# Kernel optimization log

Hardware: AMD Instinct MI355X
Metric: run time of the kernel (lower is better)

The kernel has to match this reference:

```python
import jax, jax.numpy as jnp
import numpy as np

B, T, D = 8, 1024, 768
H, DH = 12, 64
E, K, DFF = 16, 2, 3072
EPS = 1e-5


def _ln(x, w, b):
    m = x.mean(-1, keepdims=True)
    v = ((x - m) ** 2).mean(-1, keepdims=True)
    return (x - m) * jax.lax.rsqrt(v + EPS) * w + b


def setup_inputs() -> dict:
    key = jax.random.key(0)
    ks = jax.random.split(key, 12)
    s = 0.02
    return {
        "x": jax.random.normal(ks[0], (B, T, D), jnp.float32),
        "ln1_w": jnp.ones((D,), jnp.float32),
        "ln1_b": jnp.zeros((D,), jnp.float32),
        "qkv_w": jax.random.normal(ks[1], (D, 3 * D), jnp.float32) * s,
        "qkv_b": jnp.zeros((3 * D,), jnp.float32),
        "proj_w": jax.random.normal(ks[2], (D, D), jnp.float32) * s,
        "proj_b": jnp.zeros((D,), jnp.float32),
        "ln2_w": jnp.ones((D,), jnp.float32),
        "ln2_b": jnp.zeros((D,), jnp.float32),
        "router_w": jax.random.normal(ks[3], (D, E), jnp.float32) * s,
        "w1": jax.random.normal(ks[4], (E, D, DFF), jnp.float32) * s,
        "b1": jnp.zeros((E, DFF), jnp.float32),
        "w2": jax.random.normal(ks[5], (E, DFF, D), jnp.float32) * s,
        "b2": jnp.zeros((E, D), jnp.float32),
    }


def _block(x, ln1_w, ln1_b, qkv_w, qkv_b, proj_w, proj_b,
           ln2_w, ln2_b, router_w, w1, b1, w2, b2):
    # --- attention ---
    h = _ln(x, ln1_w, ln1_b)
    qkv = h @ qkv_w + qkv_b                      # [B,T,3D]
    q, k, v = jnp.split(qkv, 3, axis=-1)
    q = q.reshape(B, T, H, DH).transpose(0, 2, 1, 3)
    k = k.reshape(B, T, H, DH).transpose(0, 2, 1, 3)
    v = v.reshape(B, T, H, DH).transpose(0, 2, 1, 3)
    scores = jnp.einsum("bhqd,bhkd->bhqk", q, k) / np.sqrt(DH)
    causal = jnp.tril(jnp.ones((T, T), bool))
    scores = jnp.where(causal, scores, -jnp.inf)
    attn = jax.nn.softmax(scores, axis=-1)
    y = jnp.einsum("bhqk,bhkd->bhqd", attn, v)
    y = y.transpose(0, 2, 1, 3).reshape(B, T, D)
    x = x + y @ proj_w + proj_b                  # residual 1

    # --- MoE FFN (dense all-experts, gated combine) ---
    z = _ln(x, ln2_w, ln2_b)                     # [B,T,D]
    probs = jax.nn.softmax(z @ router_w, axis=-1)  # [B,T,E]
    top_p, ix = jax.lax.top_k(probs, K)
    gate = (jax.nn.one_hot(ix, E, dtype=probs.dtype) * top_p[..., None]).sum(-2)  # [B,T,E]
    gate_e = jnp.moveaxis(gate, -1, 0)           # [E,B,T]

    def body(acc, ew):
        g, W1, B1, W2, B2 = ew
        out = jax.nn.gelu(z @ W1 + B1, approximate=False) @ W2 + B2
        return acc + g[..., None] * out, None

    yff, _ = jax.lax.scan(body, jnp.zeros_like(z), (gate_e, w1, b1, w2, b2))
    # MoELayer returns z + yff; Block adds x again (faithful double residual)
    return x + z + yff


def reference(x, ln1_w, ln1_b, qkv_w, qkv_b, proj_w, proj_b,
              ln2_w, ln2_b, router_w, w1, b1, w2, b2):
    return _block(x, ln1_w, ln1_b, qkv_w, qkv_b, proj_w, proj_b,
                  ln2_w, ln2_b, router_w, w1, b1, w2, b2)
```

## Files before the change

kernel.cpp:

```cpp
#include <hip/hip_runtime.h>
#include <math.h>

#define D_MODEL 768
#define T_SEQ   1024
#define B_BATCH 8
#define NTOK    8192
#define H_HEADS 12
#define DHEAD   64
#define NEXP    16
#define DFF     3072
#define NPAIR   16384
#define MAXT128 144
#define MAXT256 80

typedef unsigned short u16;
typedef unsigned int   u32;

typedef __attribute__((ext_vector_type(8))) short bf16x8;
typedef __attribute__((ext_vector_type(4))) float f32x4;
typedef __attribute__((ext_vector_type(4))) u32   u32x4;

__device__ __forceinline__ float bf2f(u16 u) { return __uint_as_float(((u32)u) << 16); }
__device__ __forceinline__ u16 f2bf(float f) {
    u32 u = __float_as_uint(f);
    return (u16)((u + 0x7FFFu + ((u >> 16) & 1u)) >> 16);
}

__device__ __forceinline__ void gload16(const void* g, void* l) {
    __builtin_amdgcn_global_load_lds((const __attribute__((address_space(1))) void*)g,
                                     (__attribute__((address_space(3))) void*)l, 16, 0, 0);
}

__global__ __launch_bounds__(256) void ln_kernel(const float* __restrict__ x,
                                                 const float* __restrict__ w,
                                                 const float* __restrict__ b,
                                                 u16* __restrict__ out_bf,
                                                 float* __restrict__ out_f) {
    const int row = blockIdx.x;
    const int tid = threadIdx.x;
    const float* xr = x + (size_t)row * D_MODEL;
    float v0 = xr[tid], v1 = xr[tid + 256], v2 = xr[tid + 512];
    float s = v0 + v1 + v2;
    float s2 = v0 * v0 + v1 * v1 + v2 * v2;
#pragma unroll
    for (int o = 32; o > 0; o >>= 1) { s += __shfl_down(s, o); s2 += __shfl_down(s2, o); }
    __shared__ float red[8];
    __shared__ float stats[2];
    const int wid = tid >> 6;
    if ((tid & 63) == 0) { red[wid] = s; red[4 + wid] = s2; }
    __syncthreads();
    if (tid == 0) {
        float ts = red[0] + red[1] + red[2] + red[3];
        float ts2 = red[4] + red[5] + red[6] + red[7];
        float mean = ts * (1.0f / D_MODEL);
        float var = ts2 * (1.0f / D_MODEL) - mean * mean;
        stats[0] = mean;
        stats[1] = rsqrtf(var + 1e-5f);
    }
    __syncthreads();
    const float mean = stats[0], rstd = stats[1];
    u16* orow = out_bf + (size_t)row * D_MODEL;
    float r0 = (v0 - mean) * rstd * w[tid]       + b[tid];
    float r1 = (v1 - mean) * rstd * w[tid + 256] + b[tid + 256];
    float r2 = (v2 - mean) * rstd * w[tid + 512] + b[tid + 512];
    orow[tid] = f2bf(r0); orow[tid + 256] = f2bf(r1); orow[tid + 512] = f2bf(r2);
    if (out_f) {
        float* frow = out_f + (size_t)row * D_MODEL;
        frow[tid] = r0; frow[tid + 256] = r1; frow[tid + 512] = r2;
    }
}

__global__ __launch_bounds__(256) void transpose_cvt(const float* __restrict__ src,
                                                     u16* __restrict__ dst,
                                                     int R, int C) {
    const size_t plane = (size_t)R * C;
    src += (size_t)blockIdx.z * plane;
    dst += (size_t)blockIdx.z * plane;
    __shared__ __align__(16) u16 tile[64][72];
    const int t = threadIdx.x;
    const int r0 = blockIdx.y * 64, c0 = blockIdx.x * 64;
    {
        const int lr = t >> 2, lc = (t & 3) * 16;
        const float* sp = src + (size_t)(r0 + lr) * C + c0 + lc;
        u16 tmp[16];
#pragma unroll
        for (int j = 0; j < 4; ++j) {
            f32x4 f = *(const f32x4*)(sp + j * 4);
            tmp[j * 4 + 0] = f2bf(f[0]); tmp[j * 4 + 1] = f2bf(f[1]);
            tmp[j * 4 + 2] = f2bf(f[2]); tmp[j * 4 + 3] = f2bf(f[3]);
        }
        *(u32x4*)&tile[lr][lc]     = *(const u32x4*)&tmp[0];
        *(u32x4*)&tile[lr][lc + 8] = *(const u32x4*)&tmp[8];
    }
    __syncthreads();
    {
        const int ln = t >> 2, lk0 = (t & 3) * 16;
        u16 o[16];
#pragma unroll
        for (int j = 0; j < 16; ++j) o[j] = tile[lk0 + j][ln];
        u16* d = dst + (size_t)(c0 + ln) * R + r0 + lk0;
        *(u32x4*)&d[0] = *(const u32x4*)&o[0];
        *(u32x4*)&d[8] = *(const u32x4*)&o[8];
    }
}

template <int MODE>
__global__ __launch_bounds__(512, 4) void gemm256(
    const u16* __restrict__ A, const u16* __restrict__ Bt,
    const float* __restrict__ bias, void* __restrict__ Cout,
    const float* __restrict__ resid,
    const int* __restrict__ bucket_tok, const int* __restrict__ offsets,
    const int* __restrict__ counts, const int* __restrict__ desc_e,
    const int* __restrict__ desc_r, const int* __restrict__ tile_cnt,
    int K, int N)
{
    int e = 0, r0 = 0, off = 0, ne = 0, row0 = 0;
    const int col0 = blockIdx.x * 128;
    if constexpr (MODE >= 2) {
        if ((int)blockIdx.y >= *tile_cnt) return;
        e = desc_e[blockIdx.y];
        r0 = desc_r[blockIdx.y];
        off = offsets[e];
        ne = counts[e];
    } else {
        row0 = blockIdx.y * 256;
    }
    if constexpr (MODE == 2) Bt += (size_t)e * D_MODEL * DFF;
    if constexpr (MODE == 3) Bt += (size_t)e * DFF * D_MODEL;

    __shared__ __align__(16) u16 As[256 * 64];
    __shared__ __align__(16) u16 Bs[128 * 64];

    const int tid = threadIdx.x;
    const int lane = tid & 63;
    const int w = tid >> 6;
    const int wm = w >> 1, wn = w & 1;
    const int fr = lane & 15, fg = lane >> 4;

    const int koff = ((((tid & 7) * 16) ^ (((tid >> 3) & 7) << 4)) >> 1);

    u32 aoff[4];
#pragma unroll
    for (int i = 0; i < 4; ++i) {
        const int r = i * 64 + (tid >> 3);
        u32 row;
        if constexpr (MODE == 2) {
            int rb = r0 + r;
            row = (u32)bucket_tok[off + (rb < ne ? rb : 0)];
        } else if constexpr (MODE == 3) {
            int rb = r0 + r;
            row = (u32)(off + (rb < ne ? rb : (ne - 1)));
        } else {
            row = (u32)(row0 + r);
        }
        aoff[i] = row * (u32)K + (u32)koff;
    }
    u32 boff[2];
#pragma unroll
    for (int i = 0; i < 2; ++i) {
        const int n = i * 64 + (tid >> 3);
        boff[i] = (u32)(col0 + n) * (u32)K + (u32)koff;
    }

    f32x4 acc[4][4] = {};

    for (int k0 = 0; k0 < K; k0 += 64) {
        __syncthreads();
#pragma unroll
        for (int i = 0; i < 4; ++i)
            gload16(A + aoff[i] + k0, &As[(i * 512 + w * 64) * 8]);
#pragma unroll
        for (int i = 0; i < 2; ++i)
            gload16(Bt + boff[i] + k0, &Bs[(i * 512 + w * 64) * 8]);
        __syncthreads();
#pragma unroll
        for (int kk = 0; kk < 2; ++kk) {
            const int sw = ((kk * 64 + fg * 16) ^ ((fr & 7) << 4)) >> 1;
            bf16x8 a[4], b[4];
#pragma unroll
            for (int mi = 0; mi < 4; ++mi)
                a[mi] = *(const bf16x8*)&As[(wm * 64 + mi * 16 + fr) * 64 + sw];
#pragma unroll
            for (int ni = 0; ni < 4; ++ni)
                b[ni] = *(const bf16x8*)&Bs[(wn * 64 + ni * 16 + fr) * 64 + sw];
#pragma unroll
            for (int mi = 0; mi < 4; ++mi)
#pragma unroll
                for (int ni = 0; ni < 4; ++ni)
                    acc[mi][ni] = __builtin_amdgcn_mfma_f32_16x16x32_bf16(a[mi], b[ni], acc[mi][ni], 0, 0, 0);
        }
    }

#pragma unroll
    for (int mi = 0; mi < 4; ++mi) {
#pragma unroll
        for (int ni = 0; ni < 4; ++ni) {
            const int lr = wm * 64 + mi * 16 + fg * 4;
            const int col = col0 + wn * 64 + ni * 16 + fr;
#pragma unroll
            for (int i = 0; i < 4; ++i) {
                float v = acc[mi][ni][i];
                if constexpr (MODE == 0) {
                    int grow = row0 + lr + i;
                    ((u16*)Cout)[(size_t)grow * N + col] = f2bf(v + bias[col]);
                } else if constexpr (MODE == 1) {
                    int grow = row0 + lr + i;
                    size_t idx = (size_t)grow * N + col;
                    ((float*)Cout)[idx] = resid[idx] + v + bias[col];
                } else if constexpr (MODE == 2) {
                    int rb = r0 + lr + i;
                    if (rb < ne) {
                        float vb = v + bias[(size_t)e * DFF + col];
                        float g = 0.5f * vb * (1.0f + erff(vb * 0.70710678118654752f));
                        ((u16*)Cout)[(size_t)(off + rb) * N + col] = f2bf(g);
                    }
                } else {
                    int rb = r0 + lr + i;
                    if (rb < ne) {
                        ((float*)Cout)[(size_t)(off + rb) * N + col] = v + bias[(size_t)e * D_MODEL + col];
                    }
                }
            }
        }
    }
}

template <int MODE>
__global__ __launch_bounds__(256) void gemm128f(
    const u16* __restrict__ A, const float* __restrict__ Bf,
    const float* __restrict__ bias, void* __restrict__ Cout,
    const float* __restrict__ resid,
    const int* __restrict__ bucket_tok, const int* __restrict__ offsets,
    const int* __restrict__ counts, const int* __restrict__ desc_e,
    const int* __restrict__ desc_r, const int* __restrict__ tile_cnt,
    int K, int N)
{
    int e = 0, r0 = 0, off = 0, ne = 0, row0 = 0;
    const int col0 = blockIdx.x * 128;
    if constexpr (MODE >= 2) {
        if ((int)blockIdx.y >= *tile_cnt) return;
        e = desc_e[blockIdx.y]; r0 = desc_r[blockIdx.y];
        off = offsets[e]; ne = counts[e];
    } else row0 = blockIdx.y * 128;
    if constexpr (MODE == 2) Bf += (size_t)e * D_MODEL * DFF;
    if constexpr (MODE == 3) Bf += (size_t)e * DFF * D_MODEL;

    __shared__ __align__(16) u16 AsL[128 * 32];
    __shared__ __align__(16) u16 BsL[128 * 32];

    const int tid = threadIdx.x;
    const int lane = tid & 63;
    const int w = tid >> 6;
    const int wr = (w >> 1) * 64, wc = (w & 1) * 64;
    const int fr = lane & 15, fg = lane >> 4;
    const int lrow = lane >> 2, lk = (lane & 3) * 8;

    const u16* ag[2];
#pragma unroll
    for (int i = 0; i < 2; ++i) {
        int r = i * 64 + w * 16 + lrow;
        size_t srow;
        if constexpr (MODE == 2) {
            int rb = r0 + r;
            int tok = bucket_tok[off + (rb < ne ? rb : 0)];
            srow = (size_t)tok * K;
        } else if constexpr (MODE == 3) {
            int rb = r0 + r;
            int pp = off + (rb < ne ? rb : (ne - 1));
            srow = (size_t)pp * K;
        } else srow = (size_t)(row0 + r) * K;
        ag[i] = A + srow + lk;
    }

    f32x4 acc[4][4] = {};
    for (int k0 = 0; k0 < K; k0 += 32) {
        __syncthreads();
        gload16(ag[0] + k0, &AsL[0 * 2048 + w * 512]);
        gload16(ag[1] + k0, &AsL[1 * 2048 + w * 512]);
#pragma unroll
        for (int i = 0; i < 4; ++i) {
            int s = tid + 256 * i;
            int kk = s >> 5, n4 = (s & 31) * 4;
            f32x4 f = *(const f32x4*)(Bf + (size_t)(k0 + kk) * N + col0 + n4);
            BsL[(n4 + 0) * 32 + kk] = f2bf(f[0]);
            BsL[(n4 + 1) * 32 + kk] = f2bf(f[1]);
            BsL[(n4 + 2) * 32 + kk] = f2bf(f[2]);
            BsL[(n4 + 3) * 32 + kk] = f2bf(f[3]);
        }
        __syncthreads();
        bf16x8 a[4], b[4];
#pragma unroll
        for (int mi = 0; mi < 4; ++mi)
            a[mi] = *(const bf16x8*)&AsL[(wr + mi * 16 + fr) * 32 + fg * 8];
#pragma unroll
        for (int ni = 0; ni < 4; ++ni)
            b[ni] = *(const bf16x8*)&BsL[(wc + ni * 16 + fr) * 32 + fg * 8];
#pragma unroll
        for (int mi = 0; mi < 4; ++mi)
#pragma unroll
            for (int ni = 0; ni < 4; ++ni)
                acc[mi][ni] = __builtin_amdgcn_mfma_f32_16x16x32_bf16(a[mi], b[ni], acc[mi][ni], 0, 0, 0);
    }
#pragma unroll
    for (int mi = 0; mi < 4; ++mi) {
#pragma unroll
        for (int ni = 0; ni < 4; ++ni) {
            const int lr = wr + mi * 16 + fg * 4;
            const int col = col0 + wc + ni * 16 + fr;
#pragma unroll
            for (int i = 0; i < 4; ++i) {
                float v = acc[mi][ni][i];
                if constexpr (MODE == 0) {
                    int grow = row0 + lr + i;
                    ((u16*)Cout)[(size_t)grow * N + col] = f2bf(v + bias[col]);
                } else if constexpr (MODE == 1) {
                    int grow = row0 + lr + i;
                    size_t idx = (size_t)grow * N + col;
                    ((float*)Cout)[idx] = resid[idx] + v + bias[col];
                } else if constexpr (MODE == 2) {
                    int rb = r0 + lr + i;
                    if (rb < ne) {
                        float vb = v + bias[(size_t)e * DFF + col];
                        float g = 0.5f * vb * (1.0f + erff(vb * 0.70710678118654752f));
                        ((u16*)Cout)[(size_t)(off + rb) * N + col] = f2bf(g);
                    }
                } else {
                    int rb = r0 + lr + i;
                    if (rb < ne) {
                        ((float*)Cout)[(size_t)(off + rb) * N + col] = v + bias[(size_t)e * D_MODEL + col];
                    }
                }
            }
        }
    }
}

__global__ __launch_bounds__(256) void attn_mfma(const u16* __restrict__ qkv,
                                                 u16* __restrict__ y) {
    const int bh = blockIdx.x;
    const int b = bh / H_HEADS, h = bh % H_HEADS;
    const int qt = gridDim.y - 1 - blockIdx.y;
    const int tid = threadIdx.x, lane = tid & 63, w = tid >> 6;
    const int fr = lane & 15, fg = lane >> 4;

    __shared__ __align__(16) u16 Ks[64][72];
    __shared__ __align__(16) u16 Vt[64][72];
    __shared__ __align__(16) u16 Ps[4][16][72];

    const int tb = b * T_SEQ + qt * 64;

    bf16x8 aq[2];
    {
        const u16* qp = qkv + (size_t)(tb + w * 16 + fr) * (3 * D_MODEL) + h * DHEAD + fg * 8;
        aq[0] = *(const bf16x8*)qp;
        aq[1] = *(const bf16x8*)(qp + 32);
    }
    f32x4 accO[4] = {};
    float m_[4], l_[4];
#pragma unroll
    for (int i = 0; i < 4; ++i) { m_[i] = -1e30f; l_[i] = 0.0f; }

    for (int kt = 0; kt <= qt; ++kt) {
        __syncthreads();
        {
            const int krow = tid >> 2, c16 = (tid & 3) * 16;
            const u16* kp = qkv + (size_t)(b * T_SEQ + kt * 64 + krow) * (3 * D_MODEL)
                          + D_MODEL + h * DHEAD + c16;
            *(u32x4*)&Ks[krow][c16]     = *(const u32x4*)kp;
            *(u32x4*)&Ks[krow][c16 + 8] = *(const u32x4*)(kp + 8);
            const u16* vp = kp + D_MODEL;
            u16 vv[16];
            *(u32x4*)&vv[0] = *(const u32x4*)vp;
            *(u32x4*)&vv[8] = *(const u32x4*)(vp + 8);
#pragma unroll
            for (int j = 0; j < 16; ++j) Vt[c16 + j][krow] = vv[j];
        }
        __syncthreads();

        f32x4 s4[4] = {};
#pragma unroll
        for (int kk = 0; kk < 2; ++kk) {
#pragma unroll
            for (int ni = 0; ni < 4; ++ni) {
                bf16x8 bk = *(const bf16x8*)&Ks[ni * 16 + fr][kk * 32 + fg * 8];
                s4[ni] = __builtin_amdgcn_mfma_f32_16x16x32_bf16(aq[kk], bk, s4[ni], 0, 0, 0);
            }
        }

        const bool diag = (kt == qt);
        float p[4][4];
#pragma unroll
        for (int i = 0; i < 4; ++i) {
            const int rloc = w * 16 + fg * 4 + i;
            float rmax = -1e30f;
#pragma unroll
            for (int ni = 0; ni < 4; ++ni) {
                float v = s4[ni][i] * 0.125f;
                if (diag && (ni * 16 + fr) > rloc) v = -1e30f;
                p[ni][i] = v;
                rmax = fmaxf(rmax, v);
            }
#pragma unroll
            for (int msk = 1; msk < 16; msk <<= 1) rmax = fmaxf(rmax, __shfl_xor(rmax, msk));
            const float mn = fmaxf(m_[i], rmax);
            float sum = 0.0f;
#pragma unroll
            for (int ni = 0; ni < 4; ++ni) {
                float ev = __expf(p[ni][i] - mn);
                p[ni][i] = ev;
                sum += ev;
            }
#pragma unroll
            for (int msk = 1; msk < 16; msk <<= 1) sum += __shfl_xor(sum, msk);
            const float sc = __expf(m_[i] - mn);
            l_[i] = l_[i] * sc + sum;
            m_[i] = mn;
#pragma unroll
            for (int ni = 0; ni < 4; ++ni) accO[ni][i] *= sc;
        }

#pragma unroll
        for (int i = 0; i < 4; ++i)
#pragma unroll
            for (int ni = 0; ni < 4; ++ni)
                Ps[w][fg * 4 + i][ni * 16 + fr] = f2bf(p[ni][i]);

#pragma unroll
        for (int kk = 0; kk < 2; ++kk) {
            bf16x8 ap = *(const bf16x8*)&Ps[w][fr][kk * 32 + fg * 8];
#pragma unroll
            for (int ni = 0; ni < 4; ++ni) {
                bf16x8 bv = *(const bf16x8*)&Vt[ni * 16 + fr][kk * 32 + fg * 8];
                accO[ni] = __builtin_amdgcn_mfma_f32_16x16x32_bf16(ap, bv, accO[ni], 0, 0, 0);
            }
        }
    }

#pragma unroll
    for (int i = 0; i < 4; ++i) {
        const float inv = 1.0f / l_[i];
        u16* yp = y + (size_t)(tb + w * 16 + fg * 4 + i) * D_MODEL + h * DHEAD;
#pragma unroll
        for (int ni = 0; ni < 4; ++ni) yp[ni * 16 + fr] = f2bf(accO[ni][i] * inv);
    }
}

__global__ __launch_bounds__(64) void router_kernel(const float* __restrict__ z,
                                                    const float* __restrict__ rw,
                                                    float* __restrict__ gates,
                                                    int* __restrict__ eidx) {
    const int t = blockIdx.x;
    const int lane = threadIdx.x;
    const int e = lane & 15, part = lane >> 4;
    const float* zr = z + (size_t)t * D_MODEL;
    float acc = 0.0f;
    for (int d = part * 192; d < part * 192 + 192; ++d)
        acc += zr[d] * rw[d * NEXP + e];
    acc += __shfl_down(acc, 32);
    acc += __shfl_down(acc, 16);
    const float lg = acc;
    float logit[NEXP];
#pragma unroll
    for (int ee = 0; ee < NEXP; ++ee) logit[ee] = __shfl(lg, ee);
    if (lane == 0) {
        float m1 = -1e30f, m2 = -1e30f; int i1 = 0, i2 = 0;
#pragma unroll
        for (int ee = 0; ee < NEXP; ++ee) {
            float v = logit[ee];
            if (v > m1) { m2 = m1; i2 = i1; m1 = v; i1 = ee; }
            else if (v > m2) { m2 = v; i2 = ee; }
        }
        float den = 0.0f;
#pragma unroll
        for (int ee = 0; ee < NEXP; ++ee) den += __expf(logit[ee] - m1);
        const float inv = 1.0f / den;
        gates[2 * t] = inv;
        gates[2 * t + 1] = __expf(m2 - m1) * inv;
        eidx[2 * t] = i1;
        eidx[2 * t + 1] = i2;
    }
}

__global__ __launch_bounds__(256) void count_kernel(const int* __restrict__ eidx, int* counts) {
    int i = blockIdx.x * 256 + threadIdx.x;
    if (i < NPAIR) atomicAdd(&counts[eidx[i]], 1);
}

__global__ void offsets_kernel(const int* __restrict__ counts, int* offsets, int* cursor,
                               int* desc_e, int* desc_r, int* tile_cnt, int step) {
    if (threadIdx.x == 0 && blockIdx.x == 0) {
        int off = 0, nt = 0;
        for (int e = 0; e < NEXP; ++e) {
            offsets[e] = off;
            cursor[e] = off;
            int c = counts[e];
            for (int r = 0; r < c; r += step) { desc_e[nt] = e; desc_r[nt] = r; ++nt; }
            off += c;
        }
        *tile_cnt = nt;
    }
}

__global__ __launch_bounds__(256) void scatter_kernel(const int* __restrict__ eidx, int* cursor,
                                                      int* __restrict__ btok, int* __restrict__ ppos) {
    int i = blockIdx.x * 256 + threadIdx.x;
    if (i < NPAIR) {
        int pos = atomicAdd(&cursor[eidx[i]], 1);
        btok[pos] = i >> 1;
        ppos[i] = pos;
    }
}

__global__ __launch_bounds__(256) void final_kernel(const float* __restrict__ x1,
                                                    const float* __restrict__ zf,
                                                    const float* __restrict__ moe_o,
                                                    const float* __restrict__ gates,
                                                    const int* __restrict__ ppos,
                                                    float* __restrict__ out) {
    const int t = blockIdx.x;
    const int d = blockIdx.y * 256 + threadIdx.x;
    const size_t idx = (size_t)t * D_MODEL + d;
    const float g0 = gates[2 * t], g1 = gates[2 * t + 1];
    const int p0 = ppos[2 * t], p1 = ppos[2 * t + 1];
    out[idx] = x1[idx] + zf[idx] + g0 * moe_o[(size_t)p0 * D_MODEL + d]
                                 + g1 * moe_o[(size_t)p1 * D_MODEL + d];
}

extern "C" void kernel_launch(void* const* d_in, const int* in_sizes, int n_in,
                              void* d_out, int out_size, void* d_ws, size_t ws_size,
                              hipStream_t stream) {
    const float* x        = (const float*)d_in[0];
    const float* ln1_w    = (const float*)d_in[1];
    const float* ln1_b    = (const float*)d_in[2];
    const float* qkv_w    = (const float*)d_in[3];
    const float* qkv_b    = (const float*)d_in[4];
    const float* proj_w   = (const float*)d_in[5];
    const float* proj_b   = (const float*)d_in[6];
    const float* ln2_w    = (const float*)d_in[7];
    const float* ln2_b    = (const float*)d_in[8];
    const float* router_w = (const float*)d_in[9];
    const float* w1       = (const float*)d_in[10];
    const float* b1       = (const float*)d_in[11];
    const float* w2       = (const float*)d_in[12];
    const float* b2       = (const float*)d_in[13];
    float* out = (float*)d_out;

    char* ws = (char*)d_ws;
    size_t off = 0;
    auto alloc = [&](size_t bytes) -> void* {
        void* p = ws + off;
        off += (bytes + 255) & ~(size_t)255;
        return p;
    };
    u16*  h_bf   = (u16*)alloc((size_t)NTOK * D_MODEL * 2);
    u16*  qkv_bf = (u16*)alloc((size_t)NTOK * 3 * D_MODEL * 2);
    u16*  y_bf   = h_bf;
    float* x1    = (float*)alloc((size_t)NTOK * D_MODEL * 4);
    u16*  z_bf   = (u16*)alloc((size_t)NTOK * D_MODEL * 2);
    float* z_f   = (float*)alloc((size_t)NTOK * D_MODEL * 4);
    u16*  act    = (u16*)alloc((size_t)NPAIR * DFF * 2);
    float* moe_o = (float*)alloc((size_t)NPAIR * D_MODEL * 4);
    float* gates = (float*)alloc((size_t)NTOK * 2 * 4);
    int*  eidx   = (int*)alloc((size_t)NTOK * 2 * 4);
    int*  ppos   = (int*)alloc((size_t)NTOK * 2 * 4);
    int*  btok   = (int*)alloc((size_t)NPAIR * 4);
    int*  counts = (int*)alloc(NEXP * 4);
    int*  offs   = (int*)alloc(NEXP * 4);
    int*  cursor = (int*)alloc(NEXP * 4);
    int*  desc_e = (int*)alloc(MAXT128 * 4);
    int*  desc_r = (int*)alloc(MAXT128 * 4);
    int*  tcnt   = (int*)alloc(4);
    u16* qkvT  = (u16*)alloc((size_t)(3 * D_MODEL) * D_MODEL * 2);
    u16* projT = (u16*)alloc((size_t)D_MODEL * D_MODEL * 2);
    u16* w1t   = (u16*)alloc((size_t)NEXP * DFF * D_MODEL * 2);
    u16* w2t   = (u16*)alloc((size_t)NEXP * D_MODEL * DFF * 2);
    const bool useT = (off <= ws_size);
    (void)in_sizes; (void)n_in; (void)out_size;

    hipMemsetAsync(counts, 0, NEXP * 4, stream);

    if (useT) {
        transpose_cvt<<<dim3(3 * D_MODEL / 64, D_MODEL / 64, 1), 256, 0, stream>>>(qkv_w, qkvT, D_MODEL, 3 * D_MODEL);
        transpose_cvt<<<dim3(D_MODEL / 64, D_MODEL / 64, 1), 256, 0, stream>>>(proj_w, projT, D_MODEL, D_MODEL);
        transpose_cvt<<<dim3(DFF / 64, D_MODEL / 64, NEXP), 256, 0, stream>>>(w1, w1t, D_MODEL, DFF);
        transpose_cvt<<<dim3(D_MODEL / 64, DFF / 64, NEXP), 256, 0, stream>>>(w2, w2t, DFF, D_MODEL);
    }

    ln_kernel<<<NTOK, 256, 0, stream>>>(x, ln1_w, ln1_b, h_bf, nullptr);
    if (useT)
        gemm256<0><<<dim3(18, 32), 512, 0, stream>>>(h_bf, qkvT, qkv_b, qkv_bf, nullptr,
            nullptr, nullptr, nullptr, nullptr, nullptr, nullptr, D_MODEL, 3 * D_MODEL);
    else
        gemm128f<0><<<dim3(18, 64), 256, 0, stream>>>(h_bf, qkv_w, qkv_b, qkv_bf, nullptr,
            nullptr, nullptr, nullptr, nullptr, nullptr, nullptr, D_MODEL, 3 * D_MODEL);

    attn_mfma<<<dim3(B_BATCH * H_HEADS, T_SEQ / 64), 256, 0, stream>>>(qkv_bf, y_bf);

    if (useT)
        gemm256<1><<<dim3(6, 32), 512, 0, stream>>>(y_bf, projT, proj_b, x1, x,
            nullptr, nullptr, nullptr, nullptr, nullptr, nullptr, D_MODEL, D_MODEL);
    else
        gemm128f<1><<<dim3(6, 64), 256, 0, stream>>>(y_bf, proj_w, proj_b, x1, x,
            nullptr, nullptr, nullptr, nullptr, nullptr, nullptr, D_MODEL, D_MODEL);

    ln_kernel<<<NTOK, 256, 0, stream>>>(x1, ln2_w, ln2_b, z_bf, z_f);
    router_kernel<<<NTOK, 64, 0, stream>>>(z_f, router_w, gates, eidx);
    count_kernel<<<NPAIR / 256, 256, 0, stream>>>(eidx, counts);
    offsets_kernel<<<1, 64, 0, stream>>>(counts, offs, cursor, desc_e, desc_r, tcnt,
                                         useT ? 256 : 128);
    scatter_kernel<<<NPAIR / 256, 256, 0, stream>>>(eidx, cursor, btok, ppos);

    if (useT) {
        gemm256<2><<<dim3(DFF / 128, MAXT256), 512, 0, stream>>>(z_bf, w1t, b1, act, nullptr,
            btok, offs, counts, desc_e, desc_r, tcnt, D_MODEL, DFF);
        gemm256<3><<<dim3(D_MODEL / 128, MAXT256), 512, 0, stream>>>(act, w2t, b2, moe_o, nullptr,
            btok, offs, counts, desc_e, desc_r, tcnt, DFF, D_MODEL);
    } else {
        gemm128f<2><<<dim3(DFF / 128, MAXT128), 256, 0, stream>>>(z_bf, w1, b1, act, nullptr,
            btok, offs, counts, desc_e, desc_r, tcnt, D_MODEL, DFF);
        gemm128f<3><<<dim3(D_MODEL / 128, MAXT128), 256, 0, stream>>>(act, w2, b2, moe_o, nullptr,
            btok, offs, counts, desc_e, desc_r, tcnt, DFF, D_MODEL);
    }

    final_kernel<<<dim3(NTOK, 3), 256, 0, stream>>>(x1, z_f, moe_o, gates, ppos, out);
}
```

Baseline: 699.0 us.

## Enlarge attention query tile to 128 rows and use tanh-form GELU

```diff
diff --git a/kernel.cpp b/kernel.cpp
--- a/kernel.cpp
+++ b/kernel.cpp
@@ -24,6 +24,11 @@
 __device__ __forceinline__ u16 f2bf(float f) {
     u32 u = __float_as_uint(f);
     return (u16)((u + 0x7FFFu + ((u >> 16) & 1u)) >> 16);
+}
+
+__device__ __forceinline__ float fast_gelu(float v) {
+    float u2 = -1.5957691216f * v * (1.0f + 0.044715f * v * v);
+    return v / (1.0f + __expf(u2));
 }
 
 __device__ __forceinline__ void gload16(const void* g, void* l) {
@@ -211,8 +216,7 @@
                     int rb = r0 + lr + i;
                     if (rb < ne) {
                         float vb = v + bias[(size_t)e * DFF + col];
-                        float g = 0.5f * vb * (1.0f + erff(vb * 0.70710678118654752f));
-                        ((u16*)Cout)[(size_t)(off + rb) * N + col] = f2bf(g);
+                        ((u16*)Cout)[(size_t)(off + rb) * N + col] = f2bf(fast_gelu(vb));
                     }
                 } else {
                     int rb = r0 + lr + i;
@@ -321,8 +325,7 @@
                     int rb = r0 + lr + i;
                     if (rb < ne) {
                         float vb = v + bias[(size_t)e * DFF + col];
-                        float g = 0.5f * vb * (1.0f + erff(vb * 0.70710678118654752f));
-                        ((u16*)Cout)[(size_t)(off + rb) * N + col] = f2bf(g);
+                        ((u16*)Cout)[(size_t)(off + rb) * N + col] = f2bf(fast_gelu(vb));
                     }
                 } else {
                     int rb = r0 + lr + i;
@@ -345,22 +348,27 @@
 
     __shared__ __align__(16) u16 Ks[64][72];
     __shared__ __align__(16) u16 Vt[64][72];
-    __shared__ __align__(16) u16 Ps[4][16][72];
-
-    const int tb = b * T_SEQ + qt * 64;
-
-    bf16x8 aq[2];
-    {
-        const u16* qp = qkv + (size_t)(tb + w * 16 + fr) * (3 * D_MODEL) + h * DHEAD + fg * 8;
-        aq[0] = *(const bf16x8*)qp;
-        aq[1] = *(const bf16x8*)(qp + 32);
-    }
-    f32x4 accO[4] = {};
-    float m_[4], l_[4];
-#pragma unroll
-    for (int i = 0; i < 4; ++i) { m_[i] = -1e30f; l_[i] = 0.0f; }
-
-    for (int kt = 0; kt <= qt; ++kt) {
+    __shared__ __align__(16) u16 Ps[4][32][72];
+
+    const int tb = b * T_SEQ + qt * 128;
+    const int wrow = w * 32;
+
+    bf16x8 aq[2][2];
+#pragma unroll
+    for (int rg = 0; rg < 2; ++rg) {
+        const u16* qp = qkv + (size_t)(tb + wrow + rg * 16 + fr) * (3 * D_MODEL) + h * DHEAD + fg * 8;
+        aq[rg][0] = *(const bf16x8*)qp;
+        aq[rg][1] = *(const bf16x8*)(qp + 32);
+    }
+    f32x4 accO[2][4] = {};
+    float m_[2][4], l_[2][4];
+#pragma unroll
+    for (int rg = 0; rg < 2; ++rg)
+#pragma unroll
+        for (int i = 0; i < 4; ++i) { m_[rg][i] = -1e30f; l_[rg][i] = 0.0f; }
+
+    const int ktmax = 2 * qt + 1;
+    for (int kt = 0; kt <= ktmax; ++kt) {
         __syncthreads();
         {
             const int krow = tid >> 2, c16 = (tid & 3) * 16;
@@ -377,71 +385,77 @@
         }
         __syncthreads();
 
-        f32x4 s4[4] = {};
-#pragma unroll
-        for (int kk = 0; kk < 2; ++kk) {
-#pragma unroll
-            for (int ni = 0; ni < 4; ++ni) {
-                bf16x8 bk = *(const bf16x8*)&Ks[ni * 16 + fr][kk * 32 + fg * 8];
-                s4[ni] = __builtin_amdgcn_mfma_f32_16x16x32_bf16(aq[kk], bk, s4[ni], 0, 0, 0);
+        if (kt * 64 > qt * 128 + wrow + 31) continue;
+
+#pragma unroll
+        for (int rg = 0; rg < 2; ++rg) {
+            f32x4 s4[4] = {};
+#pragma unroll
+            for (int kk = 0; kk < 2; ++kk) {
+#pragma unroll
+                for (int ni = 0; ni < 4; ++ni) {
+                    bf16x8 bk = *(const bf16x8*)&Ks[ni * 16 + fr][kk * 32 + fg * 8];
+                    s4[ni] = __builtin_amdgcn_mfma_f32_16x16x32_bf16(aq[rg][kk], bk, s4[ni], 0, 0, 0);
+                }
             }
-        }
-
-        const bool diag = (kt == qt);
-        float p[4][4];
+            float p[4][4];
+#pragma unroll
+            for (int i = 0; i < 4; ++i) {
+                const int grow = qt * 128 + wrow + rg * 16 + fg * 4 + i;
+                float rmax = -1e30f;
+#pragma unroll
+                for (int ni = 0; ni < 4; ++ni) {
+                    float v = s4[ni][i] * 0.125f;
+                    if (kt * 64 + ni * 16 + fr > grow) v = -1e30f;
+                    p[ni][i] = v;
+                    rmax = fmaxf(rmax, v);
+                }
+#pragma unroll
+                for (int msk = 1; msk < 16; msk <<= 1) rmax = fmaxf(rmax, __shfl_xor(rmax, msk));
+                const float mn = fmaxf(m_[rg][i], rmax);
+                float sum = 0.0f;
+#pragma unroll
+                for (int ni = 0; ni < 4; ++ni) {
+                    float ev = __expf(p[ni][i] - mn);
+                    p[ni][i] = ev;
+                    sum += ev;
+                }
+#pragma unroll
+                for (int msk = 1; msk < 16; msk <<= 1) sum += __shfl_xor(sum, msk);
+                const float sc = __expf(m_[rg][i] - mn);
+                l_[rg][i] = l_[rg][i] * sc + sum;
+                m_[rg][i] = mn;
+#pragma unroll
+                for (int ni = 0; ni < 4; ++ni) accO[rg][ni][i] *= sc;
+#pragma unroll
+                for (int ni = 0; ni < 4; ++ni)
+                    Ps[w][rg * 16 + fg * 4 + i][ni * 16 + fr] = f2bf(p[ni][i]);
+            }
+        }
+
+#pragma unroll
+        for (int rg = 0; rg < 2; ++rg) {
+#pragma unroll
+            for (int kk = 0; kk < 2; ++kk) {
+                bf16x8 ap = *(const bf16x8*)&Ps[w][rg * 16 + fr][kk * 32 + fg * 8];
+#pragma unroll
+                for (int ni = 0; ni < 4; ++ni) {
+                    bf16x8 bv = *(const bf16x8*)&Vt[ni * 16 + fr][kk * 32 + fg * 8];
+                    accO[rg][ni] = __builtin_amdgcn_mfma_f32_16x16x32_bf16(ap, bv, accO[rg][ni], 0, 0, 0);
+                }
+            }
+        }
+    }
+
+#pragma unroll
+    for (int rg = 0; rg < 2; ++rg) {
 #pragma unroll
         for (int i = 0; i < 4; ++i) {
-            const int rloc = w * 16 + fg * 4 + i;
-            float rmax = -1e30f;
-#pragma unroll
-            for (int ni = 0; ni < 4; ++ni) {
-                float v = s4[ni][i] * 0.125f;
-                if (diag && (ni * 16 + fr) > rloc) v = -1e30f;
-                p[ni][i] = v;
-                rmax = fmaxf(rmax, v);
-            }
-#pragma unroll
-            for (int msk = 1; msk < 16; msk <<= 1) rmax = fmaxf(rmax, __shfl_xor(rmax, msk));
-            const float mn = fmaxf(m_[i], rmax);
-            float sum = 0.0f;
-#pragma unroll
-            for (int ni = 0; ni < 4; ++ni) {
-                float ev = __expf(p[ni][i] - mn);
-                p[ni][i] = ev;
-                sum += ev;
-            }
-#pragma unroll
-            for (int msk = 1; msk < 16; msk <<= 1) sum += __shfl_xor(sum, msk);
-            const float sc = __expf(m_[i] - mn);
-            l_[i] = l_[i] * sc + sum;
-            m_[i] = mn;
-#pragma unroll
-            for (int ni = 0; ni < 4; ++ni) accO[ni][i] *= sc;
-        }
-
-#pragma unroll
-        for (int i = 0; i < 4; ++i)
-#pragma unroll
-            for (int ni = 0; ni < 4; ++ni)
-                Ps[w][fg * 4 + i][ni * 16 + fr] = f2bf(p[ni][i]);
-
-#pragma unroll
-        for (int kk = 0; kk < 2; ++kk) {
-            bf16x8 ap = *(const bf16x8*)&Ps[w][fr][kk * 32 + fg * 8];
-#pragma unroll
-            for (int ni = 0; ni < 4; ++ni) {
-                bf16x8 bv = *(const bf16x8*)&Vt[ni * 16 + fr][kk * 32 + fg * 8];
-                accO[ni] = __builtin_amdgcn_mfma_f32_16x16x32_bf16(ap, bv, accO[ni], 0, 0, 0);
-            }
-        }
-    }
-
-#pragma unroll
-    for (int i = 0; i < 4; ++i) {
-        const float inv = 1.0f / l_[i];
-        u16* yp = y + (size_t)(tb + w * 16 + fg * 4 + i) * D_MODEL + h * DHEAD;
-#pragma unroll
-        for (int ni = 0; ni < 4; ++ni) yp[ni * 16 + fr] = f2bf(accO[ni][i] * inv);
+            const float inv = 1.0f / l_[rg][i];
+            u16* yp = y + (size_t)(tb + wrow + rg * 16 + fg * 4 + i) * D_MODEL + h * DHEAD;
+#pragma unroll
+            for (int ni = 0; ni < 4; ++ni) yp[ni * 16 + fr] = f2bf(accO[rg][ni][i] * inv);
+        }
     }
 }
 
@@ -594,7 +608,7 @@
         gemm128f<0><<<dim3(18, 64), 256, 0, stream>>>(h_bf, qkv_w, qkv_b, qkv_bf, nullptr,
             nullptr, nullptr, nullptr, nullptr, nullptr, nullptr, D_MODEL, 3 * D_MODEL);
 
-    attn_mfma<<<dim3(B_BATCH * H_HEADS, T_SEQ / 64), 256, 0, stream>>>(qkv_bf, y_bf);
+    attn_mfma<<<dim3(B_BATCH * H_HEADS, T_SEQ / 128), 256, 0, stream>>>(qkv_bf, y_bf);
 
     if (useT)
         gemm256<1><<<dim3(6, 32), 512, 0, stream>>>(y_bf, projT, proj_b, x1, x,
```

Result: no change. 697.4 us (-0.2%).
